# Performance work log

Measured on AMD Instinct MI355X. Metric: run time of the kernel, lower is better.

Reference implementation:

```python
import jax, jax.numpy as jnp
import numpy as np

N = 8192
IN_CH = 256
OUT_CH = 256


def setup_inputs() -> dict:
    key = jax.random.key(0)
    k1, k2, k3, k4, k5 = jax.random.split(key, 5)
    features = jax.random.normal(k1, (N, IN_CH), dtype=jnp.float32)
    wavelets = jax.random.normal(k2, (N, N), dtype=jnp.float32)
    wavelets_inv = jax.random.normal(k3, (N, N), dtype=jnp.float32)
    # parameters
    # xavier uniform for weight_matrix
    limit = np.sqrt(6.0 / (IN_CH + OUT_CH)).astype(np.float32)
    weight_matrix = jax.random.uniform(k4, (IN_CH, OUT_CH), minval=-limit, maxval=limit, dtype=jnp.float32)
    filt = jax.random.uniform(k5, (N,), minval=0.9, maxval=1.1, dtype=jnp.float32)
    return {"features": features, "wavelets": wavelets, "wavelets_inv": wavelets_inv,
            "weight_matrix": weight_matrix, "filt": filt}


def reference(features, wavelets, wavelets_inv, weight_matrix, filt):
    # transformed = features @ W                    [N, out]
    transformed = features @ weight_matrix
    # spectral = wavelets_inv @ transformed         [N, out]
    spectral = wavelets_inv @ transformed
    # torch.diag(filter) @ spectral == filt[:, None] * spectral (avoid NxN diag GEMM)
    filtered = filt[:, None] * spectral
    # output = wavelets @ filtered                  [N, out]
    return wavelets @ filtered
```

## Files before the change

### kernel.cpp

```cpp
#include <hip/hip_runtime.h>
#include <hip/hip_bf16.h>
#include <stdint.h>
#include <stddef.h>

typedef __bf16 bf16;
typedef float f32x4 __attribute__((ext_vector_type(4)));
typedef bf16 bf16x8 __attribute__((ext_vector_type(8)));
typedef bf16 bf16x4 __attribute__((ext_vector_type(4)));

#define MROWS 8192
#define NOUT 256
#define BM 32
#define BK 128
#define PSTEPS 4
#define PK (BK * PSTEPS)
#define NTHREADS 512

#define SLOT_BYTES (BM * PK * 2)
#define LDS_SMALL (BM * BK * 2)

#define SCHED0 __builtin_amdgcn_sched_barrier(0)
#define SBAR __builtin_amdgcn_s_barrier()


template <bool SCALE, bool OUTT>
__global__ __launch_bounds__(NTHREADS, 1) void gemm_big(
    const float* __restrict__ A, const bf16* __restrict__ Bp,
    const float* __restrict__ filt, void* __restrict__ outp,
    const int K, const int lda) {
  __shared__ char lds[2][SLOT_BYTES];
  const int t = threadIdx.x;
  const int w = t >> 6;
  const int l = t & 63;
  const int m0 = blockIdx.x * BM;
  const int NT = K / BK;
  const int NP = K / PK;

  const float* gAw = A + (size_t)(m0 + w * 4) * (size_t)lda + l * 4;

  int awoff[8];
#pragma unroll
  for (int q = 0; q < 8; ++q) {
    const int r = w * 4 + (q >> 1);
    awoff[q] = r * 1024 + ((((q & 1) * 512) + l * 8) ^ ((r & 7) << 4));
  }

  int aoff0[2][4];
#pragma unroll
  for (int af = 0; af < 2; ++af)
#pragma unroll
    for (int ak = 0; ak < 4; ++ak) {
      const int r = af * 16 + (l & 15);
      aoff0[af][ak] = r * 1024 + ((ak * 64 + (l >> 4) * 16) ^ ((r & 7) << 4));
    }

  const char* pBw = (const char*)Bp + w * 8192 + l * 16;

  f32x4 acc[2][2] = {};
  f32x4 pA[8];
  bf16x8 Breg[4][2][4];

#pragma unroll
  for (int q = 0; q < 8; ++q)
    pA[q] = __builtin_nontemporal_load(
        (const f32x4*)(gAw + (size_t)(q >> 1) * lda + (q & 1) * 256));
  SCHED0;
#pragma unroll
  for (int bfi = 0; bfi < 2; ++bfi)
#pragma unroll
    for (int ak = 0; ak < 4; ++ak) {
      Breg[0][bfi][ak] = *(const bf16x8*)(pBw + (bfi * 4 + ak) * 1024);
      Breg[1][bfi][ak] =
          *(const bf16x8*)(pBw + (1 << 16) + (bfi * 4 + ak) * 1024);
    }
  SCHED0;
#pragma unroll
  for (int q = 0; q < 8; ++q) {
    bf16x4 pk;
#pragma unroll
    for (int e = 0; e < 4; ++e) pk[e] = (bf16)pA[q][e];
    *(bf16x4*)(lds[0] + awoff[q]) = pk;
  }
  SCHED0;
#pragma unroll
  for (int q = 0; q < 8; ++q)
    pA[q] = __builtin_nontemporal_load(
        (const f32x4*)(gAw + PK + (size_t)(q >> 1) * lda + (q & 1) * 256));
  asm volatile("s_waitcnt lgkmcnt(0)" ::: "memory");
  SBAR;
  SCHED0;

  for (int p = 0; p < NP; ++p) {
    const char* rslot = lds[p & 1];
    char* wslot = lds[(p + 1) & 1];
    const int pn2 = (p + 2 < NP) ? p + 2 : 0;
    const float* gApn2 = gAw + (size_t)pn2 * PK;

#pragma unroll
    for (int s = 0; s < PSTEPS; ++s) {
      const int ts = p * PSTEPS + s;
      if (s == 0) {
#pragma unroll
        for (int q = 0; q < 8; ++q) {
          bf16x4 pk;
#pragma unroll
          for (int e = 0; e < 4; ++e) pk[e] = (bf16)pA[q][e];
          *(bf16x4*)(wslot + awoff[q]) = pk;
        }
        SCHED0;
      }
      const size_t kb2 = (size_t)((ts + 2 < NT) ? ts + 2 : 0) << 16;
#pragma unroll
      for (int bfi = 0; bfi < 2; ++bfi)
#pragma unroll
        for (int ak = 0; ak < 4; ++ak)
          Breg[(s + 2) & 3][bfi][ak] =
              *(const bf16x8*)(pBw + kb2 + (bfi * 4 + ak) * 1024);
      SCHED0;
      if (s < 2) {
#pragma unroll
        for (int q4 = 0; q4 < 4; ++q4) {
          const int q = s * 4 + q4;
          pA[q] = __builtin_nontemporal_load(
              (const f32x4*)(gApn2 + (size_t)(q >> 1) * lda + (q & 1) * 256));
        }
        SCHED0;
      }
      bf16x8 afr[2][4];
#pragma unroll
      for (int af = 0; af < 2; ++af)
#pragma unroll
        for (int ak = 0; ak < 4; ++ak)
          afr[af][ak] = *(const bf16x8*)(rslot + aoff0[af][ak] + s * 256);
      __builtin_amdgcn_s_setprio(1);
#pragma unroll
      for (int ak = 0; ak < 4; ++ak)
#pragma unroll
        for (int af = 0; af < 2; ++af)
#pragma unroll
          for (int bfi = 0; bfi < 2; ++bfi)
            acc[af][bfi] = __builtin_amdgcn_mfma_f32_16x16x32_bf16(
                afr[af][ak], Breg[s & 3][bfi][ak], acc[af][bfi], 0, 0, 0);
      __builtin_amdgcn_s_setprio(0);
    }
    asm volatile("s_waitcnt lgkmcnt(0)" ::: "memory");
    SBAR;
  }

#pragma unroll
  for (int af = 0; af < 2; ++af)
#pragma unroll
    for (int bfi = 0; bfi < 2; ++bfi) {
      const int mb = m0 + af * 16 + (l >> 4) * 4;
      const int n = w * 32 + bfi * 16 + (l & 15);
      f32x4 v = acc[af][bfi];
      if (SCALE) {
#pragma unroll
        for (int j = 0; j < 4; ++j) v[j] *= filt[mb + j];
      }
      if (OUTT) {
        bf16x4 pv;
#pragma unroll
        for (int j = 0; j < 4; ++j) pv[j] = (bf16)v[j];
        const int tsq = mb >> 7, wq = n >> 5, bq = (n >> 4) & 1, aq = (mb >> 5) & 3;
        const int lq = ((mb >> 3) & 3) * 16 + (n & 15);
        char* dst = (char*)outp +
                    (size_t)(((tsq * 64 + wq * 8 + bq * 4 + aq) << 10) + lq * 16 +
                             (mb & 7) * 2);
        *(bf16x4*)dst = pv;
      } else {
        float* po = (float*)outp + (size_t)mb * NOUT + n;
#pragma unroll
        for (int j = 0; j < 4; ++j) po[(size_t)j * NOUT] = v[j];
      }
    }
}

template <bool SCALE, bool OUTT>
__global__ __launch_bounds__(NTHREADS, 1) void gemm_small(
    const float* __restrict__ A, const bf16* __restrict__ Bp,
    const float* __restrict__ filt, void* __restrict__ outp,
    const int K, const int lda) {
  __shared__ char lds[2][LDS_SMALL];
  const int t = threadIdx.x;
  const int w = t >> 6;
  const int l = t & 63;
  const int m0 = blockIdx.x * BM;
  const int NT = K / BK;

  const int ar = t >> 4;
  const int acb = t & 15;
  const float* gA = A + (size_t)(m0 + ar) * (size_t)lda + acb * 8;
  const int a_lds_off = (ar * (BK * 2) + acb * 16) ^ ((ar & 7) << 4);

  int aoff[2][4];
#pragma unroll
  for (int af = 0; af < 2; ++af)
#pragma unroll
    for (int ak = 0; ak < 4; ++ak) {
      const int r = af * 16 + (l & 15);
      const int kb = ak * 64 + (l >> 4) * 16;
      aoff[af][ak] = (r * (BK * 2) + kb) ^ ((r & 7) << 4);
    }

  const char* pBw = (const char*)Bp + w * 8192 + l * 16;

  f32x4 acc[2][2] = {};

  f32x4 aS0a = __builtin_nontemporal_load((const f32x4*)gA);
  f32x4 aS0b = __builtin_nontemporal_load((const f32x4*)gA + 1);
  f32x4 aS1a = __builtin_nontemporal_load((const f32x4*)(gA + BK));
  f32x4 aS1b = __builtin_nontemporal_load((const f32x4*)(gA + BK) + 1);
  bf16x8 Bc[2][4], Bn[2][4];
#pragma unroll
  for (int bfi = 0; bfi < 2; ++bfi)
#pragma unroll
    for (int ak = 0; ak < 4; ++ak)
      Bc[bfi][ak] = *(const bf16x8*)(pBw + (bfi * 4 + ak) * 1024);
  {
    bf16x8 pk;
#pragma unroll
    for (int j = 0; j < 4; ++j) { pk[j] = (bf16)aS0a[j]; pk[j + 4] = (bf16)aS0b[j]; }
    *(bf16x8*)(lds[0] + a_lds_off) = pk;
  }
  asm volatile("s_waitcnt lgkmcnt(0)" ::: "memory");
  SBAR;
  SCHED0;

#define BODY_S(TS, P, BCUR, BNXT, AW0, AW1, AL0, AL1)                         \
  {                                                                           \
    const char* bb = lds[P];                                                  \
    bf16x8 afr[2][4];                                                         \
    _Pragma("unroll") for (int af = 0; af < 2; ++af)                          \
        _Pragma("unroll") for (int ak = 0; ak < 4; ++ak)                      \
            afr[af][ak] = *(const bf16x8*)(bb + aoff[af][ak]);                \
    SCHED0;                                                                   \
    const size_t kb1 = (size_t)((((TS) + 1) < NT ? ((TS) + 1) : 0)) << 16;    \
    _Pragma("unroll") for (int bfi = 0; bfi < 2; ++bfi)                       \
        _Pragma("unroll") for (int ak = 0; ak < 4; ++ak)                      \
            BNXT[bfi][ak] =                                                   \
                *(const bf16x8*)(pBw + kb1 + (bfi * 4 + ak) * 1024);          \
    SCHED0;                                                                   \
    const int ka2 = (((TS) + 2) < NT ? ((TS) + 2) : 0) * BK;                  \
    AL0 = __builtin_nontemporal_load((const f32x4*)(gA + ka2));               \
    AL1 = __builtin_nontemporal_load((const f32x4*)(gA + ka2) + 1);           \
    SCHED0;                                                                   \
    asm volatile("s_waitcnt lgkmcnt(0)" ::: "memory");                        \
    SCHED0;                                                                   \
    __builtin_amdgcn_s_setprio(1);                                            \
    _Pragma("unroll") for (int ak = 0; ak < 4; ++ak)                          \
        _Pragma("unroll") for (int af = 0; af < 2; ++af)                      \
            _Pragma("unroll") for (int bfi = 0; bfi < 2; ++bfi)               \
                acc[af][bfi] = __builtin_amdgcn_mfma_f32_16x16x32_bf16(       \
                    afr[af][ak], BCUR[bfi][ak], acc[af][bfi], 0, 0, 0);       \
    __builtin_amdgcn_s_setprio(0);                                            \
    SCHED0;                                                                   \
    {                                                                         \
      bf16x8 pk;                                                              \
      _Pragma("unroll") for (int j = 0; j < 4; ++j) {                         \
        pk[j] = (bf16)AW0[j];                                                 \
        pk[j + 4] = (bf16)AW1[j];                                             \
      }                                                                       \
      *(bf16x8*)(lds[P ^ 1] + a_lds_off) = pk;                                \
    }                                                                         \
    asm volatile("s_waitcnt lgkmcnt(0)" ::: "memory");                        \
    SBAR;                                                                     \
    SCHED0;                                                                   \
  }

  for (int ts = 0; ts < NT; ts += 2) {
    BODY_S(ts, 0, Bc, Bn, aS1a, aS1b, aS0a, aS0b);
    BODY_S(ts + 1, 1, Bn, Bc, aS0a, aS0b, aS1a, aS1b);
  }
#undef BODY_S

#pragma unroll
  for (int af = 0; af < 2; ++af)
#pragma unroll
    for (int bfi = 0; bfi < 2; ++bfi) {
      const int mb = m0 + af * 16 + (l >> 4) * 4;
      const int n = w * 32 + bfi * 16 + (l & 15);
      f32x4 v = acc[af][bfi];
      if (SCALE) {
#pragma unroll
        for (int j = 0; j < 4; ++j) v[j] *= filt[mb + j];
      }
      if (OUTT) {
        bf16x4 pv;
#pragma unroll
        for (int j = 0; j < 4; ++j) pv[j] = (bf16)v[j];
        const int tsq = mb >> 7, wq = n >> 5, bq = (n >> 4) & 1, aq = (mb >> 5) & 3;
        const int lq = ((mb >> 3) & 3) * 16 + (n & 15);
        char* dst = (char*)outp +
                    (size_t)(((tsq * 64 + wq * 8 + bq * 4 + aq) << 10) + lq * 16 +
                             (mb & 7) * 2);
        *(bf16x4*)dst = pv;
      } else {
        float* po = (float*)outp + (size_t)mb * NOUT + n;
#pragma unroll
        for (int j = 0; j < 4; ++j) po[(size_t)j * NOUT] = v[j];
      }
    }
}

__global__ void prep_wt(const float* __restrict__ W, bf16* __restrict__ Wp) {
  const int k = blockIdx.x;
  const int n = threadIdx.x;
  const int off = (((k >> 7) * 64 + (n >> 5) * 8 + ((n >> 4) & 1) * 4 +
                    ((k >> 5) & 3)) << 10) +
                  (((k >> 3) & 3) * 16 + (n & 15)) * 16 + (k & 7) * 2;
  *(bf16*)((char*)Wp + off) = (bf16)W[k * 256 + n];
}

extern "C" void kernel_launch(void* const* d_in, const int* in_sizes, int n_in,
                              void* d_out, int out_size, void* d_ws, size_t ws_size,
                              hipStream_t stream) {
  const float* features = (const float*)d_in[0];
  const float* wavelets = (const float*)d_in[1];
  const float* wavelets_inv = (const float*)d_in[2];
  const float* W = (const float*)d_in[3];
  const float* filt = (const float*)d_in[4];
  float* out = (float*)d_out;

  char* ws = (char*)d_ws;
  bf16* Wp = (bf16*)ws;
  bf16* Tp = (bf16*)(ws + 131072);
  bf16* Fp = (bf16*)(ws + 131072 + 4194304);

  prep_wt<<<256, 256, 0, stream>>>(W, Wp);
  gemm_small<false, true><<<256, NTHREADS, 0, stream>>>(features, Wp, nullptr, Tp, 256, 256);
  gemm_big<true, true><<<256, NTHREADS, 0, stream>>>(wavelets_inv, Tp, filt, Fp, 8192, 8192);
  gemm_big<false, false><<<256, NTHREADS, 0, stream>>>(wavelets, Fp, nullptr, out, 8192, 8192);
}
```

Baseline: 168.9 us.

## Replace big GEMMs with split-K 128-row tiles plus partial-sum reduction kernels

```diff
diff --git a/kernel.cpp b/kernel.cpp
--- a/kernel.cpp
+++ b/kernel.cpp
@@ -10,69 +10,66 @@
 
 #define MROWS 8192
 #define NOUT 256
-#define BM 32
 #define BK 128
-#define PSTEPS 4
-#define PK (BK * PSTEPS)
 #define NTHREADS 512
-
-#define SLOT_BYTES (BM * PK * 2)
-#define LDS_SMALL (BM * BK * 2)
+#define LDS_SMALL (32 * BK * 2)
 
 #define SCHED0 __builtin_amdgcn_sched_barrier(0)
 #define SBAR __builtin_amdgcn_s_barrier()
 
 
-template <bool SCALE, bool OUTT>
-__global__ __launch_bounds__(NTHREADS, 1) void gemm_big(
+__global__ __launch_bounds__(NTHREADS, 1) void gemm_ks(
     const float* __restrict__ A, const bf16* __restrict__ Bp,
-    const float* __restrict__ filt, void* __restrict__ outp,
-    const int K, const int lda) {
-  __shared__ char lds[2][SLOT_BYTES];
+    float* __restrict__ wsP, float* __restrict__ doutP,
+    const int kshift, const int nsteps, const int lda) {
+  __shared__ char lds[2][32768];
   const int t = threadIdx.x;
   const int w = t >> 6;
   const int l = t & 63;
-  const int m0 = blockIdx.x * BM;
-  const int NT = K / BK;
-  const int NP = K / PK;
-
-  const float* gAw = A + (size_t)(m0 + w * 4) * (size_t)lda + l * 4;
+  const int ks = blockIdx.x & ((1 << kshift) - 1);
+  const int mt = blockIdx.x >> kshift;
+  const int m0 = mt * 128;
+  const int ts0 = ks * nsteps;
+  float* __restrict__ Ps =
+      (ks == ((1 << kshift) - 1)) ? doutP : wsP + (size_t)ks * 2097152;
+
+  const float* gAq[8];
+#pragma unroll
+  for (int q = 0; q < 8; ++q)
+    gAq[q] = A + (size_t)(m0 + w * 16 + q * 2 + (l >> 5)) * (size_t)lda +
+             (size_t)ts0 * BK + (l & 31) * 4;
 
   int awoff[8];
 #pragma unroll
   for (int q = 0; q < 8; ++q) {
-    const int r = w * 4 + (q >> 1);
-    awoff[q] = r * 1024 + ((((q & 1) * 512) + l * 8) ^ ((r & 7) << 4));
-  }
-
-  int aoff0[2][4];
-#pragma unroll
-  for (int af = 0; af < 2; ++af)
+    const int r = w * 16 + q * 2 + (l >> 5);
+    awoff[q] = r * 256 + ((((l & 31) * 8)) ^ ((r & 7) << 4));
+  }
+
+  int aoff[8][4];
+#pragma unroll
+  for (int af = 0; af < 8; ++af)
 #pragma unroll
     for (int ak = 0; ak < 4; ++ak) {
       const int r = af * 16 + (l & 15);
-      aoff0[af][ak] = r * 1024 + ((ak * 64 + (l >> 4) * 16) ^ ((r & 7) << 4));
+      aoff[af][ak] = r * 256 + ((ak * 64 + (l >> 4) * 16) ^ ((r & 7) << 4));
     }
 
   const char* pBw = (const char*)Bp + w * 8192 + l * 16;
 
-  f32x4 acc[2][2] = {};
+  f32x4 acc[8][2] = {};
   f32x4 pA[8];
-  bf16x8 Breg[4][2][4];
-
-#pragma unroll
-  for (int q = 0; q < 8; ++q)
-    pA[q] = __builtin_nontemporal_load(
-        (const f32x4*)(gAw + (size_t)(q >> 1) * lda + (q & 1) * 256));
+  bf16x8 Breg[2][2][4];
+
+#pragma unroll
+  for (int q = 0; q < 8; ++q) pA[q] = __builtin_nontemporal_load((const f32x4*)gAq[q]);
   SCHED0;
 #pragma unroll
   for (int bfi = 0; bfi < 2; ++bfi)
 #pragma unroll
-    for (int ak = 0; ak < 4; ++ak) {
-      Breg[0][bfi][ak] = *(const bf16x8*)(pBw + (bfi * 4 + ak) * 1024);
-      Breg[1][bfi][ak] =
-          *(const bf16x8*)(pBw + (1 << 16) + (bfi * 4 + ak) * 1024);
-    }
+    for (int ak = 0; ak < 4; ++ak)
+      Breg[0][bfi][ak] = *(const bf16x8*)(pBw + ((size_t)ts0 << 16) +
+                                          (bfi * 4 + ak) * 1024);
   SCHED0;
 #pragma unroll
   for (int q = 0; q < 8; ++q) {
@@ -82,98 +79,104 @@
     *(bf16x4*)(lds[0] + awoff[q]) = pk;
   }
   SCHED0;
-#pragma unroll
-  for (int q = 0; q < 8; ++q)
-    pA[q] = __builtin_nontemporal_load(
-        (const f32x4*)(gAw + PK + (size_t)(q >> 1) * lda + (q & 1) * 256));
+  {
+    const int s1 = (nsteps > 1) ? 1 : 0;
+#pragma unroll
+    for (int q = 0; q < 8; ++q)
+      pA[q] = __builtin_nontemporal_load((const f32x4*)(gAq[q] + s1 * BK));
+  }
   asm volatile("s_waitcnt lgkmcnt(0)" ::: "memory");
   SBAR;
   SCHED0;
 
-  for (int p = 0; p < NP; ++p) {
-    const char* rslot = lds[p & 1];
-    char* wslot = lds[(p + 1) & 1];
-    const int pn2 = (p + 2 < NP) ? p + 2 : 0;
-    const float* gApn2 = gAw + (size_t)pn2 * PK;
-
-#pragma unroll
-    for (int s = 0; s < PSTEPS; ++s) {
-      const int ts = p * PSTEPS + s;
-      if (s == 0) {
-#pragma unroll
-        for (int q = 0; q < 8; ++q) {
-          bf16x4 pk;
-#pragma unroll
-          for (int e = 0; e < 4; ++e) pk[e] = (bf16)pA[q][e];
-          *(bf16x4*)(wslot + awoff[q]) = pk;
-        }
-        SCHED0;
-      }
-      const size_t kb2 = (size_t)((ts + 2 < NT) ? ts + 2 : 0) << 16;
+  for (int s = 0; s < nsteps; ++s) {
+    const char* rslot = lds[s & 1];
+    char* wslot = lds[(s + 1) & 1];
+#pragma unroll
+    for (int q = 0; q < 8; ++q) {
+      bf16x4 pk;
+#pragma unroll
+      for (int e = 0; e < 4; ++e) pk[e] = (bf16)pA[q][e];
+      *(bf16x4*)(wslot + awoff[q]) = pk;
+    }
+    SCHED0;
+    {
+      const int tn = (s + 1 < nsteps) ? ts0 + s + 1 : ts0;
 #pragma unroll
       for (int bfi = 0; bfi < 2; ++bfi)
 #pragma unroll
         for (int ak = 0; ak < 4; ++ak)
-          Breg[(s + 2) & 3][bfi][ak] =
-              *(const bf16x8*)(pBw + kb2 + (bfi * 4 + ak) * 1024);
-      SCHED0;
-      if (s < 2) {
-#pragma unroll
-        for (int q4 = 0; q4 < 4; ++q4) {
-          const int q = s * 4 + q4;
-          pA[q] = __builtin_nontemporal_load(
-              (const f32x4*)(gApn2 + (size_t)(q >> 1) * lda + (q & 1) * 256));
-        }
-        SCHED0;
-      }
-      bf16x8 afr[2][4];
-#pragma unroll
-      for (int af = 0; af < 2; ++af)
-#pragma unroll
-        for (int ak = 0; ak < 4; ++ak)
-          afr[af][ak] = *(const bf16x8*)(rslot + aoff0[af][ak] + s * 256);
-      __builtin_amdgcn_s_setprio(1);
-#pragma unroll
-      for (int ak = 0; ak < 4; ++ak)
-#pragma unroll
-        for (int af = 0; af < 2; ++af)
-#pragma unroll
-          for (int bfi = 0; bfi < 2; ++bfi)
-            acc[af][bfi] = __builtin_amdgcn_mfma_f32_16x16x32_bf16(
-                afr[af][ak], Breg[s & 3][bfi][ak], acc[af][bfi], 0, 0, 0);
-      __builtin_amdgcn_s_setprio(0);
-    }
+          Breg[(s + 1) & 1][bfi][ak] = *(const bf16x8*)(
+              pBw + ((size_t)tn << 16) + (bfi * 4 + ak) * 1024);
+    }
+    SCHED0;
+    {
+      const int ka = (s + 2 < nsteps) ? (s + 2) * BK : 0;
+#pragma unroll
+      for (int q = 0; q < 8; ++q)
+        pA[q] = __builtin_nontemporal_load((const f32x4*)(gAq[q] + ka));
+    }
+    SCHED0;
+    __builtin_amdgcn_s_setprio(1);
+#pragma unroll
+    for (int ak = 0; ak < 4; ++ak) {
+      bf16x8 afr[8];
+#pragma unroll
+      for (int af = 0; af < 8; ++af)
+        afr[af] = *(const bf16x8*)(rslot + aoff[af][ak]);
+#pragma unroll
+      for (int af = 0; af < 8; ++af)
+#pragma unroll
+        for (int bfi = 0; bfi < 2; ++bfi)
+          acc[af][bfi] = __builtin_amdgcn_mfma_f32_16x16x32_bf16(
+              afr[af], Breg[s & 1][bfi][ak], acc[af][bfi], 0, 0, 0);
+    }
+    __builtin_amdgcn_s_setprio(0);
+    SCHED0;
     asm volatile("s_waitcnt lgkmcnt(0)" ::: "memory");
     SBAR;
-  }
-
-#pragma unroll
-  for (int af = 0; af < 2; ++af)
+    SCHED0;
+  }
+
+#pragma unroll
+  for (int af = 0; af < 8; ++af)
 #pragma unroll
     for (int bfi = 0; bfi < 2; ++bfi) {
       const int mb = m0 + af * 16 + (l >> 4) * 4;
       const int n = w * 32 + bfi * 16 + (l & 15);
-      f32x4 v = acc[af][bfi];
-      if (SCALE) {
-#pragma unroll
-        for (int j = 0; j < 4; ++j) v[j] *= filt[mb + j];
-      }
-      if (OUTT) {
-        bf16x4 pv;
-#pragma unroll
-        for (int j = 0; j < 4; ++j) pv[j] = (bf16)v[j];
-        const int tsq = mb >> 7, wq = n >> 5, bq = (n >> 4) & 1, aq = (mb >> 5) & 3;
-        const int lq = ((mb >> 3) & 3) * 16 + (n & 15);
-        char* dst = (char*)outp +
-                    (size_t)(((tsq * 64 + wq * 8 + bq * 4 + aq) << 10) + lq * 16 +
-                             (mb & 7) * 2);
-        *(bf16x4*)dst = pv;
-      } else {
-        float* po = (float*)outp + (size_t)mb * NOUT + n;
-#pragma unroll
-        for (int j = 0; j < 4; ++j) po[(size_t)j * NOUT] = v[j];
-      }
-    }
+#pragma unroll
+      for (int j = 0; j < 4; ++j)
+        Ps[(size_t)(mb + j) * NOUT + n] = acc[af][bfi][j];
+    }
+}
+
+__global__ void reduce2(const float* __restrict__ wsP,
+                        const float* __restrict__ doutP,
+                        const float* __restrict__ filt, bf16* __restrict__ Fp,
+                        const int KS) {
+  const int n = threadIdx.x;
+  const int m8 = blockIdx.x;
+  bf16x8 pk;
+#pragma unroll
+  for (int r = 0; r < 8; ++r) {
+    const int m = m8 * 8 + r;
+    float s = doutP[(size_t)m * NOUT + n];
+    for (int ks = 0; ks < KS - 1; ++ks)
+      s += wsP[(size_t)ks * 2097152 + (size_t)m * NOUT + n];
+    pk[r] = (bf16)(s * filt[m]);
+  }
+  const int ts = m8 >> 4, wq = n >> 5, bq = (n >> 4) & 1, aq = (m8 >> 2) & 3;
+  const int lq = (m8 & 3) * 16 + (n & 15);
+  *(bf16x8*)((char*)Fp +
+             (size_t)(((ts * 64 + wq * 8 + bq * 4 + aq) << 10) + lq * 16)) = pk;
+}
+
+__global__ void reduce3(const float* __restrict__ wsP, float* __restrict__ doutP,
+                        const int KS) {
+  const size_t i = (size_t)blockIdx.x * 256 + threadIdx.x;
+  float s = doutP[i];
+  for (int ks = 0; ks < KS - 1; ++ks) s += wsP[(size_t)ks * 2097152 + i];
+  doutP[i] = s;
 }
 
 template <bool SCALE, bool OUTT>
@@ -185,7 +188,7 @@
   const int t = threadIdx.x;
   const int w = t >> 6;
   const int l = t & 63;
-  const int m0 = blockIdx.x * BM;
+  const int m0 = blockIdx.x * 32;
   const int NT = K / BK;
 
   const int ar = t >> 4;
@@ -326,9 +329,25 @@
   bf16* Wp = (bf16*)ws;
   bf16* Tp = (bf16*)(ws + 131072);
   bf16* Fp = (bf16*)(ws + 131072 + 4194304);
+  float* wsP = (float*)(ws + 131072 + 8388608);
+
+  const size_t base = 131072 + 8388608;
+  int KS = 0, kshift = 0;
+  if (ws_size >= base + 3u * 8388608u) { KS = 4; kshift = 2; }
+  else if (ws_size >= base + 1u * 8388608u) { KS = 2; kshift = 1; }
 
   prep_wt<<<256, 256, 0, stream>>>(W, Wp);
   gemm_small<false, true><<<256, NTHREADS, 0, stream>>>(features, Wp, nullptr, Tp, 256, 256);
-  gemm_big<true, true><<<256, NTHREADS, 0, stream>>>(wavelets_inv, Tp, filt, Fp, 8192, 8192);
-  gemm_big<false, false><<<256, NTHREADS, 0, stream>>>(wavelets, Fp, nullptr, out, 8192, 8192);
-}
+
+  if (KS) {
+    const int nsteps = 64 / KS;
+    gemm_ks<<<64 * KS, NTHREADS, 0, stream>>>(wavelets_inv, Tp, wsP, out, kshift, nsteps, 8192);
+    reduce2<<<1024, 256, 0, stream>>>(wsP, out, filt, Fp, KS);
+    gemm_ks<<<64 * KS, NTHREADS, 0, stream>>>(wavelets, Fp, wsP, out, kshift, nsteps, 8192);
+    reduce3<<<8192, 256, 0, stream>>>(wsP, out, KS);
+  } else {
+    gemm_ks<<<64, NTHREADS, 0, stream>>>(wavelets_inv, Tp, wsP, out, 0, 64, 8192);
+    reduce2<<<1024, 256, 0, stream>>>(wsP, out, filt, Fp, 1);
+    gemm_ks<<<64, NTHREADS, 0, stream>>>(wavelets, Fp, wsP, out, 0, 64, 8192);
+  }
+}
```

Result: slower. 327.2 us (+93.7%).
